# Optimization experiments

Hardware: AMD Instinct MI355X
Metric: run time of the kernel (lower is better)

The kernel has to match this reference:

```python
import jax, jax.numpy as jnp
import numpy as np


def _conv(x, w, padding):
    # x: NCHW, w: OIHW
    return jax.lax.conv_general_dilated(
        x, w, window_strides=(1, 1), padding=padding,
        dimension_numbers=('NCHW', 'OIHW', 'NCHW'))


def setup_inputs() -> dict:
    key = jax.random.key(0)
    ks = jax.random.split(key, 4)
    B, Cin, H, W = 128, 1024, 14, 14
    planes, expansion = 256, 4
    x = jax.random.normal(ks[0], (B, Cin, H, W), dtype=jnp.float32)
    # conv weights (layouts are fully dense since rho=0.0)
    w1 = jax.random.normal(ks[1], (planes, Cin, 1, 1), dtype=jnp.float32) * 0.02
    w2 = jax.random.normal(ks[2], (planes, planes, 3, 3), dtype=jnp.float32) * 0.02
    w3 = jax.random.normal(ks[3], (planes * expansion, planes, 1, 1), dtype=jnp.float32) * 0.02
    # Fixup scalar biases / scale
    z = jnp.zeros((1,), dtype=jnp.float32)
    return {
        'x': x, 'w1': w1, 'w2': w2, 'w3': w3,
        'bias1b': z, 'bias2a': z, 'bias2b': z, 'bias3a': z, 'bias3b': z,
        'rscale': jnp.ones((1,), dtype=jnp.float32), 'rbias': z,
    }


def reference(x, w1, w2, w3, bias1b, bias2a, bias2b, bias3a, bias3b, rscale, rbias):
    # conv1(x) + bias1b  (1x1, fused output bias)
    out = _conv(x, w1, 'VALID') + bias1b[0]
    # conv2(out + bias2a) + bias2b  (3x3, pad 1, fused input+output bias)
    out = _conv(out + bias2a[0], w2, 'SAME') + bias2b[0]
    # conv3(out + bias3a) + bias3b  (1x1)
    out = _conv(out + bias3a[0], w3, 'VALID') + bias3b[0]
    # fused scale + bias + residual ReLU: relu(out*rscale + rbias + identity)
    return jax.nn.relu(out * rscale[0] + rbias[0] + x)
```

## Files before the change

kernel.cpp:

```cpp
#include <hip/hip_runtime.h>
#include <stdint.h>

typedef __bf16 bf16x8 __attribute__((ext_vector_type(8)));
typedef float f32x4 __attribute__((ext_vector_type(4)));
typedef unsigned short u16;

__device__ __forceinline__ u16 f2bf(float f){
  uint32_t u = __float_as_uint(f);
  u = (u + 0x7fffu + ((u >> 16) & 1u)) >> 16;
  return (u16)u;
}

__device__ __forceinline__ void gl_lds16(const void* g, void* l){
  __builtin_amdgcn_global_load_lds((const __attribute__((address_space(1))) void*)g,
                                   (__attribute__((address_space(3))) void*)l, 16, 0, 0);
}

__global__ void cvt_f32_bf16(const float* __restrict__ in, u16* __restrict__ out, int n){
  int i = blockIdx.x*256 + threadIdx.x;
  if (i < n) out[i] = f2bf(in[i]);
}

__global__ void prep_w2k(const float* __restrict__ in, u16* __restrict__ out){
  int i = blockIdx.x*256 + threadIdx.x;
  if (i < 589824){
    int o = i / 2304, r = i - o*2304, kq = r >> 8, c = r & 255;
    out[i] = f2bf(in[((size_t)o*256 + c)*9 + kq]);
  }
}

__global__ __launch_bounds__(256) void transform_x(const float* __restrict__ x,
                                                   u16* __restrict__ xp0){
  __shared__ float lds[64*201];
  const int b = blockIdx.y, c0 = blockIdx.x*64, t = threadIdx.x;
  const float4* src = (const float4*)x + (size_t)b*50176 + (size_t)c0*49;
  #pragma unroll
  for (int r = 0; r < 13; ++r){
    int q = r*256 + t;
    if (q < 3136){
      unsigned c = (unsigned)q / 49u, f = (unsigned)q - c*49u;
      float4 v = src[q];
      float* d = &lds[c*201 + f*4];
      d[0]=v.x; d[1]=v.y; d[2]=v.z; d[3]=v.w;
    }
  }
  __syncthreads();
  const int c4 = (t & 15)*4, pg = t >> 4;
  #pragma unroll
  for (int r = 0; r < 13; ++r){
    int p = r*16 + pg;
    if (p < 196){
      ushort4 pk;
      ((u16*)&pk)[0] = f2bf(lds[(c4+0)*201 + p]);
      ((u16*)&pk)[1] = f2bf(lds[(c4+1)*201 + p]);
      ((u16*)&pk)[2] = f2bf(lds[(c4+2)*201 + p]);
      ((u16*)&pk)[3] = f2bf(lds[(c4+3)*201 + p]);
      *(ushort4*)&xp0[((size_t)b*196 + p)*1024 + c0 + c4] = pk;
    }
  }
}

__global__ void zfill_borders(u16* __restrict__ xp1){
  int tid = blockIdx.x*256 + threadIdx.x;
  int row_i = tid >> 5, w = tid & 31;
  unsigned b = (unsigned)row_i / 60u, k = (unsigned)row_i - b*60u;
  int y, xx;
  if (k < 32){ y = (k>>4)*15; xx = k & 15; }
  else if (k < 46){ y = k - 31; xx = 0; }
  else { y = k - 45; xx = 15; }
  size_t row = (size_t)b*256 + y*16 + xx;
  ((ulonglong2*)(xp1 + row*256))[w] = (ulonglong2){0,0};
}

template<int CID>
__global__ __launch_bounds__(256, 2) void gemm_k(
    const u16* __restrict__ A, const u16* __restrict__ B,
    u16* __restrict__ Obf, float* __restrict__ Of32, const float* __restrict__ xres,
    const float* __restrict__ s0, const float* __restrict__ s1, const float* __restrict__ s2)
{
  constexpr int KTOT  = (CID==1) ? 1024 : (CID==2) ? 2304 : 256;
  constexpr int NSTEP = KTOT / 64;

  __shared__ char lds[65536];
  const int t    = threadIdx.x;
  const int lane = t & 63;
  const int w    = t >> 6;
  const int wm   = (w >> 1) * 64, wn = (w & 1) * 64;
  const int m0   = blockIdx.y * 128, n0 = blockIdx.x * 128;

  f32x4 acc[4][4] = {};

  uint32_t aoff[4], boff[4];
  #pragma unroll
  for (int i = 0; i < 4; ++i){
    int gl = i*256 + t, row = gl >> 3, ss = gl & 7;
    int xo = (ss ^ (row & 7)) << 4;
    aoff[i] = (uint32_t)(m0 + row) * (KTOT*2) + xo;
    uint32_t n = n0 + row;
    if constexpr (CID==1)      boff[i] = n * 2048u + xo;
    else if constexpr (CID==3) boff[i] = n * 512u + xo;
    else {
      uint32_t b = n / 196u, p = n - b*196u;
      uint32_t py = p / 14u,  px = p - py*14u;
      uint32_t prow = b*256u + (py+1)*16u + (px+1);
      boff[i] = prow * 512u + xo;
    }
  }

  auto stage = [&](int buf, int s){
    char* Ab = lds + buf*32768;
    char* Bb = Ab + 16384;
    const int ka = s*128;
    int kb;
    if constexpr (CID==2){
      int kq = s >> 2;
      kb = ((kq/3 - 1)*16 + (kq%3) - 1)*512 + (s & 3)*128;
    } else kb = ka;
    #pragma unroll
    for (int i = 0; i < 4; ++i){
      int gl = i*256 + t;
      gl_lds16((const char*)A + aoff[i] + ka, Ab + gl*16);
      gl_lds16((const char*)B + (int64_t)boff[i] + kb, Bb + gl*16);
    }
  };

  auto compute = [&](int buf){
    char* Ab = lds + buf*32768;
    char* Bb = Ab + 16384;
    #pragma unroll
    for (int h = 0; h < 2; ++h){
      bf16x8 af[4], bfr[4];
      #pragma unroll
      for (int i = 0; i < 4; ++i){
        int row = wm + i*16 + (lane & 15);
        af[i] = *(const bf16x8*)(Ab + row*128 + (((h*4 + (lane>>4)) ^ (row & 7)) << 4));
      }
      #pragma unroll
      for (int j = 0; j < 4; ++j){
        int row = wn + j*16 + (lane & 15);
        bfr[j] = *(const bf16x8*)(Bb + row*128 + (((h*4 + (lane>>4)) ^ (row & 7)) << 4));
      }
      #pragma unroll
      for (int i = 0; i < 4; ++i)
        #pragma unroll
        for (int j = 0; j < 4; ++j)
          acc[i][j] = __builtin_amdgcn_mfma_f32_16x16x32_bf16(af[i], bfr[j], acc[i][j], 0, 0, 0);
    }
  };

  stage(0, 0);
  __syncthreads();
  for (int s = 0; s < NSTEP; ++s){
    if (s + 1 < NSTEP) stage((s+1) & 1, s+1);
    compute(s & 1);
    __syncthreads();
  }

  if constexpr (CID==1){
    float badd = s0[0] + s1[0];
    #pragma unroll
    for (int i = 0; i < 4; ++i){
      int o = m0 + wm + i*16 + ((lane >> 4) << 2);
      #pragma unroll
      for (int j = 0; j < 4; ++j){
        uint32_t n = n0 + wn + j*16 + (lane & 15);
        uint32_t b = n / 196u, p = n - b*196u;
        uint32_t py = p / 14u, px = p - py*14u;
        size_t rn = (size_t)b*256 + (py+1)*16 + (px+1);
        ushort4 pk;
        #pragma unroll
        for (int q = 0; q < 4; ++q) ((u16*)&pk)[q] = f2bf(acc[i][j][q] + badd);
        *(ushort4*)(Obf + rn*256 + o) = pk;
      }
    }
  } else if constexpr (CID==2){
    float badd = s0[0] + s1[0];
    #pragma unroll
    for (int i = 0; i < 4; ++i){
      int o = m0 + wm + i*16 + ((lane >> 4) << 2);
      #pragma unroll
      for (int j = 0; j < 4; ++j){
        size_t n = n0 + wn + j*16 + (lane & 15);
        ushort4 pk;
        #pragma unroll
        for (int q = 0; q < 4; ++q) ((u16*)&pk)[q] = f2bf(acc[i][j][q] + badd);
        *(ushort4*)(Obf + n*256 + o) = pk;
      }
    }
  } else {
    float b3 = s0[0], rs = s1[0], rb = s2[0];
    #pragma unroll
    for (int i = 0; i < 4; ++i){
      int o = m0 + wm + i*16 + ((lane >> 4) << 2);
      #pragma unroll
      for (int j = 0; j < 4; ++j){
        uint32_t n = n0 + wn + j*16 + (lane & 15);
        uint32_t b = n / 196u, p = n - b*196u;
        size_t base = ((size_t)b*1024 + o)*196 + p;
        #pragma unroll
        for (int q = 0; q < 4; ++q){
          float v = (acc[i][j][q] + b3)*rs + rb + xres[base + (size_t)q*196];
          Of32[base + (size_t)q*196] = fmaxf(v, 0.f);
        }
      }
    }
  }
}

extern "C" void kernel_launch(void* const* d_in, const int* in_sizes, int n_in,
                              void* d_out, int out_size, void* d_ws, size_t ws_size,
                              hipStream_t stream){
  (void)in_sizes; (void)n_in; (void)out_size; (void)ws_size;
  const float* x   = (const float*)d_in[0];
  const float* w1  = (const float*)d_in[1];
  const float* w2  = (const float*)d_in[2];
  const float* w3  = (const float*)d_in[3];
  const float* b1b = (const float*)d_in[4];
  const float* b2a = (const float*)d_in[5];
  const float* b2b = (const float*)d_in[6];
  const float* b3a = (const float*)d_in[7];
  const float* b3b = (const float*)d_in[8];
  const float* rsc = (const float*)d_in[9];
  const float* rbi = (const float*)d_in[10];

  char* ws  = (char*)d_ws;
  u16*  xp1 = (u16*)ws;
  u16*  xp2 = (u16*)(ws + 16777216);
  u16*  wb1 = (u16*)(ws + 29622272);
  u16*  wb2 = (u16*)(ws + 30146560);
  u16*  wb3 = (u16*)(ws + 31326208);
  u16*  xp0 = (u16*)d_out;

  cvt_f32_bf16<<<dim3(1024), 256, 0, stream>>>(w1, wb1, 262144);
  prep_w2k    <<<dim3(2304), 256, 0, stream>>>(w2, wb2);
  cvt_f32_bf16<<<dim3(1024), 256, 0, stream>>>(w3, wb3, 262144);
  transform_x <<<dim3(16,128), 256, 0, stream>>>(x, xp0);
  zfill_borders<<<dim3(960), 256, 0, stream>>>(xp1);

  gemm_k<1><<<dim3(196, 2), 256, 0, stream>>>(wb1, xp0, xp1, nullptr, nullptr, b1b, b2a, nullptr);
  gemm_k<2><<<dim3(196, 2), 256, 0, stream>>>(wb2, xp1, xp2, nullptr, nullptr, b2b, b3a, nullptr);
  gemm_k<3><<<dim3(196, 8), 256, 0, stream>>>(wb3, xp2, nullptr, (float*)d_out, x, b3b, rsc, rbi);
}
```

Measured before the change: 339.4 us.

## Shrink conv1/conv2 N-tile, single-buffer conv3, and stage conv3 epilogue through LDS

The conv1 and conv2 GEMMs go from a 128 to a 64 N-tile, doubling the grid to 392x2 so the blocks fill the CUs better, and their occupancy hint is raised to 3. Conv3 now uses a single 33KB LDS buffer so 4 blocks can fit per CU. Its epilogue transposes the accumulators through LDS so the residual read and output write use coalesced float4 accesses instead of 196-strided scalar ones. The trade-offs are less operand reuse per block in the smaller tiles and lost load/compute overlap in conv3.

```diff
diff --git a/kernel.cpp b/kernel.cpp
--- a/kernel.cpp
+++ b/kernel.cpp
@@ -73,29 +73,40 @@
 }
 
 template<int CID>
-__global__ __launch_bounds__(256, 2) void gemm_k(
+__global__ __launch_bounds__(256, (CID==3) ? 4 : 3) void gemm_k(
     const u16* __restrict__ A, const u16* __restrict__ B,
     u16* __restrict__ Obf, float* __restrict__ Of32, const float* __restrict__ xres,
     const float* __restrict__ s0, const float* __restrict__ s1, const float* __restrict__ s2)
 {
   constexpr int KTOT  = (CID==1) ? 1024 : (CID==2) ? 2304 : 256;
   constexpr int NSTEP = KTOT / 64;
-
-  __shared__ char lds[65536];
+  constexpr int BN    = (CID==3) ? 128 : 64;
+  constexpr int WN    = (CID==3) ? 64 : 32;
+  constexpr int NJ    = WN / 16;
+  constexpr int NBG   = BN*8/256;
+  constexpr int BUFB  = 16384 + BN*128;
+  constexpr size_t LDSZ = (CID==3) ? 33792 : 2*(size_t)BUFB;
+
+  __shared__ char lds[LDSZ];
   const int t    = threadIdx.x;
   const int lane = t & 63;
   const int w    = t >> 6;
-  const int wm   = (w >> 1) * 64, wn = (w & 1) * 64;
-  const int m0   = blockIdx.y * 128, n0 = blockIdx.x * 128;
-
-  f32x4 acc[4][4] = {};
-
-  uint32_t aoff[4], boff[4];
+  const int wm   = (w >> 1) * 64, wn = (w & 1) * WN;
+  const int m0   = blockIdx.y * 128, n0 = blockIdx.x * BN;
+
+  f32x4 acc[4][NJ] = {};
+
+  uint32_t aoff[4], boff[NBG];
   #pragma unroll
   for (int i = 0; i < 4; ++i){
     int gl = i*256 + t, row = gl >> 3, ss = gl & 7;
     int xo = (ss ^ (row & 7)) << 4;
     aoff[i] = (uint32_t)(m0 + row) * (KTOT*2) + xo;
+  }
+  #pragma unroll
+  for (int i = 0; i < NBG; ++i){
+    int gl = i*256 + t, row = gl >> 3, ss = gl & 7;
+    int xo = (ss ^ (row & 7)) << 4;
     uint32_t n = n0 + row;
     if constexpr (CID==1)      boff[i] = n * 2048u + xo;
     else if constexpr (CID==3) boff[i] = n * 512u + xo;
@@ -108,7 +119,7 @@
   }
 
   auto stage = [&](int buf, int s){
-    char* Ab = lds + buf*32768;
+    char* Ab = lds + buf*BUFB;
     char* Bb = Ab + 16384;
     const int ka = s*128;
     int kb;
@@ -117,91 +128,110 @@
       kb = ((kq/3 - 1)*16 + (kq%3) - 1)*512 + (s & 3)*128;
     } else kb = ka;
     #pragma unroll
-    for (int i = 0; i < 4; ++i){
-      int gl = i*256 + t;
-      gl_lds16((const char*)A + aoff[i] + ka, Ab + gl*16);
-      gl_lds16((const char*)B + (int64_t)boff[i] + kb, Bb + gl*16);
-    }
+    for (int i = 0; i < 4; ++i)
+      gl_lds16((const char*)A + aoff[i] + ka, Ab + (i*256 + t)*16);
+    #pragma unroll
+    for (int i = 0; i < NBG; ++i)
+      gl_lds16((const char*)B + (int64_t)boff[i] + kb, Bb + (i*256 + t)*16);
   };
 
   auto compute = [&](int buf){
-    char* Ab = lds + buf*32768;
+    char* Ab = lds + buf*BUFB;
     char* Bb = Ab + 16384;
     #pragma unroll
     for (int h = 0; h < 2; ++h){
-      bf16x8 af[4], bfr[4];
+      bf16x8 af[4], bfr[NJ];
       #pragma unroll
       for (int i = 0; i < 4; ++i){
         int row = wm + i*16 + (lane & 15);
         af[i] = *(const bf16x8*)(Ab + row*128 + (((h*4 + (lane>>4)) ^ (row & 7)) << 4));
       }
       #pragma unroll
-      for (int j = 0; j < 4; ++j){
+      for (int j = 0; j < NJ; ++j){
         int row = wn + j*16 + (lane & 15);
         bfr[j] = *(const bf16x8*)(Bb + row*128 + (((h*4 + (lane>>4)) ^ (row & 7)) << 4));
       }
       #pragma unroll
       for (int i = 0; i < 4; ++i)
         #pragma unroll
-        for (int j = 0; j < 4; ++j)
+        for (int j = 0; j < NJ; ++j)
           acc[i][j] = __builtin_amdgcn_mfma_f32_16x16x32_bf16(af[i], bfr[j], acc[i][j], 0, 0, 0);
     }
   };
 
-  stage(0, 0);
-  __syncthreads();
-  for (int s = 0; s < NSTEP; ++s){
-    if (s + 1 < NSTEP) stage((s+1) & 1, s+1);
-    compute(s & 1);
+  if constexpr (CID==3){
+    #pragma unroll
+    for (int s = 0; s < NSTEP; ++s){
+      if (s) __syncthreads();
+      stage(0, s);
+      __syncthreads();
+      compute(0);
+    }
+  } else {
+    stage(0, 0);
     __syncthreads();
-  }
-
-  if constexpr (CID==1){
+    for (int s = 0; s < NSTEP; ++s){
+      if (s + 1 < NSTEP) stage((s+1) & 1, s+1);
+      compute(s & 1);
+      __syncthreads();
+    }
+  }
+
+  if constexpr (CID==1 || CID==2){
     float badd = s0[0] + s1[0];
     #pragma unroll
     for (int i = 0; i < 4; ++i){
       int o = m0 + wm + i*16 + ((lane >> 4) << 2);
       #pragma unroll
-      for (int j = 0; j < 4; ++j){
+      for (int j = 0; j < NJ; ++j){
         uint32_t n = n0 + wn + j*16 + (lane & 15);
-        uint32_t b = n / 196u, p = n - b*196u;
-        uint32_t py = p / 14u, px = p - py*14u;
-        size_t rn = (size_t)b*256 + (py+1)*16 + (px+1);
+        size_t rn;
+        if constexpr (CID==1){
+          uint32_t b = n / 196u, p = n - b*196u;
+          uint32_t py = p / 14u, px = p - py*14u;
+          rn = (size_t)b*256 + (py+1)*16 + (px+1);
+        } else rn = n;
         ushort4 pk;
         #pragma unroll
         for (int q = 0; q < 4; ++q) ((u16*)&pk)[q] = f2bf(acc[i][j][q] + badd);
         *(ushort4*)(Obf + rn*256 + o) = pk;
       }
     }
-  } else if constexpr (CID==2){
-    float badd = s0[0] + s1[0];
-    #pragma unroll
-    for (int i = 0; i < 4; ++i){
-      int o = m0 + wm + i*16 + ((lane >> 4) << 2);
-      #pragma unroll
-      for (int j = 0; j < 4; ++j){
-        size_t n = n0 + wn + j*16 + (lane & 15);
-        ushort4 pk;
+  } else {
+    float b3 = s0[0], rs = s1[0], rbv = s2[0];
+    float* ldsF = (float*)lds;
+    #pragma unroll
+    for (int pass = 0; pass < 2; ++pass){
+      __syncthreads();
+      if ((wm >> 6) == pass){
         #pragma unroll
-        for (int q = 0; q < 4; ++q) ((u16*)&pk)[q] = f2bf(acc[i][j][q] + badd);
-        *(ushort4*)(Obf + n*256 + o) = pk;
-      }
-    }
-  } else {
-    float b3 = s0[0], rs = s1[0], rb = s2[0];
-    #pragma unroll
-    for (int i = 0; i < 4; ++i){
-      int o = m0 + wm + i*16 + ((lane >> 4) << 2);
-      #pragma unroll
-      for (int j = 0; j < 4; ++j){
-        uint32_t n = n0 + wn + j*16 + (lane & 15);
+        for (int i = 0; i < 4; ++i){
+          int rb = i*16 + ((lane >> 4) << 2);
+          #pragma unroll
+          for (int j = 0; j < 4; ++j){
+            int col = wn + j*16 + (lane & 15);
+            #pragma unroll
+            for (int q = 0; q < 4; ++q) ldsF[(rb + q)*132 + col] = acc[i][j][q];
+          }
+        }
+      }
+      __syncthreads();
+      #pragma unroll
+      for (int r = 0; r < 8; ++r){
+        int row = (w << 4) + ((lane >> 5) << 3) + r;
+        int n4  = (lane & 31) << 2;
+        float4 v = *(float4*)&ldsF[row*132 + n4];
+        uint32_t n = n0 + n4;
         uint32_t b = n / 196u, p = n - b*196u;
+        int o = m0 + pass*64 + row;
         size_t base = ((size_t)b*1024 + o)*196 + p;
-        #pragma unroll
-        for (int q = 0; q < 4; ++q){
-          float v = (acc[i][j][q] + b3)*rs + rb + xres[base + (size_t)q*196];
-          Of32[base + (size_t)q*196] = fmaxf(v, 0.f);
-        }
+        float4 xr = *(const float4*)&xres[base];
+        float4 ov;
+        ov.x = fmaxf((v.x + b3)*rs + rbv + xr.x, 0.f);
+        ov.y = fmaxf((v.y + b3)*rs + rbv + xr.y, 0.f);
+        ov.z = fmaxf((v.z + b3)*rs + rbv + xr.z, 0.f);
+        ov.w = fmaxf((v.w + b3)*rs + rbv + xr.w, 0.f);
+        *(float4*)&Of32[base] = ov;
       }
     }
   }
@@ -237,7 +267,7 @@
   transform_x <<<dim3(16,128), 256, 0, stream>>>(x, xp0);
   zfill_borders<<<dim3(960), 256, 0, stream>>>(xp1);
 
-  gemm_k<1><<<dim3(196, 2), 256, 0, stream>>>(wb1, xp0, xp1, nullptr, nullptr, b1b, b2a, nullptr);
-  gemm_k<2><<<dim3(196, 2), 256, 0, stream>>>(wb2, xp1, xp2, nullptr, nullptr, b2b, b3a, nullptr);
+  gemm_k<1><<<dim3(392, 2), 256, 0, stream>>>(wb1, xp0, xp1, nullptr, nullptr, b1b, b2a, nullptr);
+  gemm_k<2><<<dim3(392, 2), 256, 0, stream>>>(wb2, xp1, xp2, nullptr, nullptr, b2b, b3a, nullptr);
   gemm_k<3><<<dim3(196, 8), 256, 0, stream>>>(wb3, xp2, nullptr, (float*)d_out, x, b3b, rsc, rbi);
 }
```

After: 341.3 us. Within noise of the previous version (+0.5%).
